# Optimization experiments

Hardware: AMD Instinct MI355X
Metric: run time of the kernel (lower is better)

## Reference

```python
import jax, jax.numpy as jnp
import numpy as np

S, B, C = 7, 2, 20          # YOLOv1 grid / boxes / classes
NE = B * 5 + C              # 30 channels per cell
BATCH = 32768
NBOX = 4                    # ground-truth boxes per image
L_COORD = 5.0


def _encode_np(boxes, classes):
    """Vectorized numpy replica of YoloLoss.encode, including its quirks:
    conf written at channel 4 + S*k (=> 4 and 11), class at channel 10 which is
    then overwritten by wh_y*S via the s+2:s+4 slice for k=1 (s=7 -> 9:11).
    boxes: [N, nb, 4] in xyxy, classes: [N, nb] int."""
    N, nb = classes.shape
    t = np.zeros((N, S, S, NE), np.float32)
    wh = boxes[:, :, 2:] - boxes[:, :, :2]
    cxcy = (boxes[:, :, 2:] + boxes[:, :, :2]) / 2.0
    cell = 1.0 / S
    ij = np.ceil(cxcy / cell) - 1.0                 # [N, nb, 2] (col, row)
    ijc = np.clip(ij, 0, S - 1).astype(np.int64)
    img = np.repeat(np.arange(N), nb)
    col = ijc[:, :, 0].ravel()
    row = ijc[:, :, 1].ravel()
    whf = (wh * S).reshape(-1, 2).astype(np.float32)
    delta = ((cxcy - ij * cell) / cell).reshape(-1, 2).astype(np.float32)
    cls = classes.ravel().astype(np.float32)
    t[img, row, col, 4] = 1.0          # conf, k=0 (4 + S*0)
    t[img, row, col, 11] = 1.0         # conf, k=1 (4 + S*1)
    t[img, row, col, 10] = cls         # class id (will be clobbered below)
    t[img, row, col, 2:4] = whf        # k=0 wh
    t[img, row, col, 0:2] = delta      # k=0 xy
    t[img, row, col, 9:11] = whf       # k=1 wh -- overwrites channel 10!
    t[img, row, col, 7:9] = delta      # k=1 xy
    return t.reshape(N, S * S, NE)


def setup_inputs() -> dict:
    key = jax.random.key(0)
    prediction = jax.random.normal(key, (BATCH, S * S, NE), dtype=jnp.float32)
    rng = np.random.default_rng(0)
    cxcy = rng.uniform(0.15, 0.85, (BATCH, NBOX, 2)).astype(np.float32)
    wh = rng.uniform(0.05, 0.3, (BATCH, NBOX, 2)).astype(np.float32)
    boxes = np.concatenate([cxcy - wh / 2, cxcy + wh / 2], axis=-1)  # xyxy
    classes = rng.integers(0, C, (BATCH, NBOX))
    target = jnp.asarray(_encode_np(boxes, classes))
    return {"prediction": prediction, "target": target}


def _point_form(b):
    # cxcywh -> xyxy on last axis
    return jnp.concatenate([b[..., :2] - b[..., 2:4] / 2,
                            b[..., :2] + b[..., 2:4] / 2], axis=-1)


def _iou(a, b):
    # a: [..., Bp, 4], b: [..., Bt, 4] (xyxy) -> [..., Bp, Bt]
    a = a[..., :, None, :]
    b = b[..., None, :, :]
    lo = jnp.maximum(a[..., :2], b[..., :2])
    hi = jnp.minimum(a[..., 2:], b[..., 2:])
    inter = jnp.prod(jnp.clip(hi - lo, 0.0, None), axis=-1)
    area_a = jnp.prod(a[..., 2:] - a[..., :2], axis=-1)
    area_b = jnp.prod(b[..., 2:] - b[..., :2], axis=-1)
    return inter / (area_a + area_b - inter + 1e-12)


def reference(prediction, target):
    coord = target[:, :, 4] > 0                         # [N, G] cells with objects
    bp = prediction[:, :, :B * 5].reshape(*prediction.shape[:2], B, 5)
    bt = target[:, :, :B * 5].reshape(*target.shape[:2], B, 5)

    # responsible-box matching: iou[bp_i, bt_j], argmax over predicted boxes per target box
    iou = _iou(_point_form(bp[..., :4]), _point_form(bt[..., :4]))  # [N,G,Bp,Bt]
    idx = jnp.argmax(iou, axis=-2)                                  # [N,G,Bt]
    resp = (jax.nn.one_hot(idx, B, dtype=jnp.float32).sum(-2) > 0)  # dedup, [N,G,B]
    resp = resp & coord[..., None]
    resp_f = resp.astype(jnp.float32)
    cnt = jnp.maximum(resp_f.sum(), 1.0)

    # containment loss: BCE-with-logits, mean over responsible boxes
    conf_p = bp[..., 4]
    conf_t = bt[..., 4]
    bce = jnp.logaddexp(0.0, conf_p) - conf_p * conf_t
    contain_loss = jnp.sum(bce * resp_f) / cnt

    # localization loss: mean MSE on xy + mean MSE on wh over responsible boxes
    sq_xy = (bp[..., 0:2] - bt[..., 0:2]) ** 2
    sq_wh = (bp[..., 2:4] - bt[..., 2:4]) ** 2
    loc_loss = (jnp.sum(sq_xy * resp_f[..., None]) / (2.0 * cnt)
                + jnp.sum(sq_wh * resp_f[..., None]) / (2.0 * cnt))

    # class loss: cross-entropy, mean over object cells
    logits = prediction[:, :, B * 5:]                               # [N,G,C]
    cls = jnp.clip(jnp.floor(target[:, :, B * 5]), 0, C - 1).astype(jnp.int32)
    lsm = jax.nn.log_softmax(logits, axis=-1)
    nll = -jnp.take_along_axis(lsm, cls[..., None], axis=-1)[..., 0]
    coord_f = coord.astype(jnp.float32)
    class_loss = jnp.sum(nll * coord_f) / jnp.maximum(coord_f.sum(), 1.0)

    # NOTE: original also computes l_noobj * noobj MSE into total_loss but then
    # returns class + contain + l_coord*loc, so noobj is dead code.
    return class_loss + contain_loss + L_COORD * loc_loss
```

## Files before the change

kernel.cpp:

```cpp
#include <hip/hip_runtime.h>
#include <math.h>

#define NCELL (32768 * 49)
#define NE 30
#define NC 20
#define G1 1568
#define BLK 256
#define CPB 1024


__device__ __forceinline__ void process_cell(
    const float* __restrict__ pred, const float* __restrict__ targ, int cell,
    float& a0, float& a1, float& a2, float& a3, float& a4, float& a5) {

    const float2* p2 = reinterpret_cast<const float2*>(pred + (size_t)cell * NE);
    const float2* t2 = reinterpret_cast<const float2*>(targ + (size_t)cell * NE);

    float p[30], t[12];
    #pragma unroll
    for (int i = 0; i < 15; ++i) { float2 v = p2[i]; p[2*i] = v.x; p[2*i+1] = v.y; }
    #pragma unroll
    for (int i = 0; i < 6; ++i)  { float2 v = t2[i]; t[2*i] = v.x; t[2*i+1] = v.y; }

    float iou[2][2];
    #pragma unroll
    for (int i = 0; i < 2; ++i) {
        const float pcx = p[5*i], pcy = p[5*i+1], pw = p[5*i+2], ph = p[5*i+3];
        const float alx = pcx - pw*0.5f, aly = pcy - ph*0.5f;
        const float ahx = pcx + pw*0.5f, ahy = pcy + ph*0.5f;
        const float area_a = pw * ph;
        #pragma unroll
        for (int j = 0; j < 2; ++j) {
            const float tcx = t[5*j], tcy = t[5*j+1], tw = t[5*j+2], th = t[5*j+3];
            const float blx = tcx - tw*0.5f, bly = tcy - th*0.5f;
            const float bhx = tcx + tw*0.5f, bhy = tcy + th*0.5f;
            float ix = fminf(ahx, bhx) - fmaxf(alx, blx);
            float iy = fminf(ahy, bhy) - fmaxf(aly, bly);
            ix = fmaxf(ix, 0.f); iy = fmaxf(iy, 0.f);
            const float inter = ix * iy;
            const float area_b = tw * th;
            iou[i][j] = inter / (area_a + area_b - inter + 1e-12f);
        }
    }
    const int idx0 = (iou[1][0] > iou[0][0]) ? 1 : 0;
    const int idx1 = (iou[1][1] > iou[0][1]) ? 1 : 0;

    #pragma unroll
    for (int k = 0; k < 2; ++k) {
        const bool resp = (idx0 == k || idx1 == k);
        if (resp) {
            a0 += 1.f;
            const float cp = p[5*k+4], ct = t[5*k+4];
            a1 += fmaxf(cp, 0.f) + log1pf(expf(-fabsf(cp))) - cp * ct;
            const float dx = p[5*k]   - t[5*k];
            const float dy = p[5*k+1] - t[5*k+1];
            a2 += dx*dx + dy*dy;
            const float dw = p[5*k+2] - t[5*k+2];
            const float dh = p[5*k+3] - t[5*k+3];
            a3 += dw*dw + dh*dh;
        }
    }

    a5 += 1.f;
    const float cf = fminf(fmaxf(floorf(t[10]), 0.f), 19.f);
    const int cls = (int)cf;
    float m = p[10];
    #pragma unroll
    for (int c = 1; c < NC; ++c) m = fmaxf(m, p[10 + c]);
    float se = 0.f;
    float sel = 0.f;
    #pragma unroll
    for (int c = 0; c < NC; ++c) {
        se += expf(p[10 + c] - m);
        sel += (c == cls) ? p[10 + c] : 0.f;
    }
    a4 += -(sel - m - logf(se));
}

__global__ __launch_bounds__(BLK) void yolo_partial(
    const float* __restrict__ pred,
    const float* __restrict__ targ,
    float* __restrict__ partial) {

    const int base = blockIdx.x * CPB;
    const int tid  = threadIdx.x;
    const int wave = tid >> 6;
    const int lane = tid & 63;

    float t4v[4];
    #pragma unroll
    for (int k = 0; k < 4; ++k)
        t4v[k] = targ[(size_t)(base + k * BLK + tid) * NE + 4];

    __shared__ int s_idx[4][256];
    __shared__ int s_cnt[4];
    int cnt = 0;
    #pragma unroll
    for (int k = 0; k < 4; ++k) {
        const bool c = t4v[k] > 0.f;
        const unsigned long long m = __ballot(c);
        const int pre = __popcll(m & ((1ull << lane) - 1ull));
        if (c) s_idx[wave][cnt + pre] = k * BLK + tid;
        cnt += __popcll(m);
    }
    if (lane == 0) s_cnt[wave] = cnt;
    __syncthreads();

    const int c0 = s_cnt[0], c1 = s_cnt[1], c2 = s_cnt[2], c3 = s_cnt[3];
    const int total = c0 + c1 + c2 + c3;

    float a0 = 0.f, a1 = 0.f, a2 = 0.f, a3 = 0.f, a4 = 0.f, a5 = 0.f;

    for (int i = tid; i < total; i += BLK) {
        int j = i, w = 0;
        if (j >= c0) { j -= c0; w = 1;
            if (j >= c1) { j -= c1; w = 2;
                if (j >= c2) { j -= c2; w = 3; } } }
        const int loc = s_idx[w][j];
        process_cell(pred, targ, base + loc, a0, a1, a2, a3, a4, a5);
    }

    #pragma unroll
    for (int off = 32; off > 0; off >>= 1) {
        a0 += __shfl_down(a0, off, 64);
        a1 += __shfl_down(a1, off, 64);
        a2 += __shfl_down(a2, off, 64);
        a3 += __shfl_down(a3, off, 64);
        a4 += __shfl_down(a4, off, 64);
        a5 += __shfl_down(a5, off, 64);
    }

    __shared__ float sm[4][6];
    if (lane == 0) {
        sm[wave][0] = a0; sm[wave][1] = a1; sm[wave][2] = a2;
        sm[wave][3] = a3; sm[wave][4] = a4; sm[wave][5] = a5;
    }
    __syncthreads();
    if (tid == 0) {
        #pragma unroll
        for (int k = 0; k < 6; ++k) {
            float s = sm[0][k] + sm[1][k] + sm[2][k] + sm[3][k];
            partial[blockIdx.x * 6 + k] = s;
        }
    }
}

__global__ __launch_bounds__(BLK) void yolo_final(
    const float* __restrict__ partial, float* __restrict__ out) {
    __shared__ double sm[BLK][6];
    double a[6] = {0, 0, 0, 0, 0, 0};
    for (int i = threadIdx.x; i < G1; i += BLK) {
        #pragma unroll
        for (int k = 0; k < 6; ++k) a[k] += (double)partial[i * 6 + k];
    }
    #pragma unroll
    for (int k = 0; k < 6; ++k) sm[threadIdx.x][k] = a[k];
    __syncthreads();
    for (int off = BLK / 2; off > 0; off >>= 1) {
        if (threadIdx.x < off) {
            #pragma unroll
            for (int k = 0; k < 6; ++k) sm[threadIdx.x][k] += sm[threadIdx.x + off][k];
        }
        __syncthreads();
    }
    if (threadIdx.x == 0) {
        const double resp_sum  = sm[0][0];
        const double bce_sum   = sm[0][1];
        const double sqxy_sum  = sm[0][2];
        const double sqwh_sum  = sm[0][3];
        const double nll_sum   = sm[0][4];
        const double coord_sum = sm[0][5];
        const double cnt = fmax(resp_sum, 1.0);
        const double contain_loss = bce_sum / cnt;
        const double loc_loss = (sqxy_sum + sqwh_sum) / (2.0 * cnt);
        const double class_loss = nll_sum / fmax(coord_sum, 1.0);
        out[0] = (float)(class_loss + contain_loss + 5.0 * loc_loss);
    }
}

extern "C" void kernel_launch(void* const* d_in, const int* in_sizes, int n_in,
                              void* d_out, int out_size, void* d_ws, size_t ws_size,
                              hipStream_t stream) {
    const float* pred = (const float*)d_in[0];
    const float* targ = (const float*)d_in[1];
    float* partial = (float*)d_ws;

    yolo_partial<<<G1, BLK, 0, stream>>>(pred, targ, partial);
    yolo_final<<<1, BLK, 0, stream>>>(partial, (float*)d_out);
}
```

Before: 49.03 us.

## Fuse final reduction into main kernel via last-block atomic counter

Merges the two-kernel partial/final reduction into one kernel: each block stores its partial sums, increments a global counter, and the last block to arrive performs the double-precision final reduction. It also halves the cells per block and doubles the grid for more parallelism and smaller shared index arrays. This removes a second kernel launch in exchange for an extra memset, an atomic per block, and a serial tail in the last block over twice as many partials.

```diff
diff --git a/kernel.cpp b/kernel.cpp
--- a/kernel.cpp
+++ b/kernel.cpp
@@ -4,9 +4,9 @@
 #define NCELL (32768 * 49)
 #define NE 30
 #define NC 20
-#define G1 1568
 #define BLK 256
-#define CPB 1024
+#define CPB 512
+#define G1 3136
 
 
 __device__ __forceinline__ void process_cell(
@@ -77,30 +77,36 @@
     a4 += -(sel - m - logf(se));
 }
 
-__global__ __launch_bounds__(BLK) void yolo_partial(
+__global__ __launch_bounds__(BLK) void yolo_fused(
     const float* __restrict__ pred,
     const float* __restrict__ targ,
-    float* __restrict__ partial) {
+    unsigned int* __restrict__ counter,
+    float* __restrict__ partial,
+    float* __restrict__ out) {
 
     const int base = blockIdx.x * CPB;
     const int tid  = threadIdx.x;
     const int wave = tid >> 6;
     const int lane = tid & 63;
 
-    float t4v[4];
-    #pragma unroll
-    for (int k = 0; k < 4; ++k)
-        t4v[k] = targ[(size_t)(base + k * BLK + tid) * NE + 4];
-
-    __shared__ int s_idx[4][256];
+    float t4a = targ[(size_t)(base + tid)       * NE + 4];
+    float t4b = targ[(size_t)(base + BLK + tid) * NE + 4];
+
+    __shared__ int s_idx[4][128];
     __shared__ int s_cnt[4];
     int cnt = 0;
-    #pragma unroll
-    for (int k = 0; k < 4; ++k) {
-        const bool c = t4v[k] > 0.f;
+    {
+        const bool c = t4a > 0.f;
         const unsigned long long m = __ballot(c);
         const int pre = __popcll(m & ((1ull << lane) - 1ull));
-        if (c) s_idx[wave][cnt + pre] = k * BLK + tid;
+        if (c) s_idx[wave][pre] = tid;
+        cnt = __popcll(m);
+    }
+    {
+        const bool c = t4b > 0.f;
+        const unsigned long long m = __ballot(c);
+        const int pre = __popcll(m & ((1ull << lane) - 1ull));
+        if (c) s_idx[wave][cnt + pre] = BLK + tid;
         cnt += __popcll(m);
     }
     if (lane == 0) s_cnt[wave] = cnt;
@@ -116,8 +122,7 @@
         if (j >= c0) { j -= c0; w = 1;
             if (j >= c1) { j -= c1; w = 2;
                 if (j >= c2) { j -= c2; w = 3; } } }
-        const int loc = s_idx[w][j];
-        process_cell(pred, targ, base + loc, a0, a1, a2, a3, a4, a5);
+        process_cell(pred, targ, base + s_idx[w][j], a0, a1, a2, a3, a4, a5);
     }
 
     #pragma unroll
@@ -131,6 +136,7 @@
     }
 
     __shared__ float sm[4][6];
+    __shared__ int s_is_last;
     if (lane == 0) {
         sm[wave][0] = a0; sm[wave][1] = a1; sm[wave][2] = a2;
         sm[wave][3] = a3; sm[wave][4] = a4; sm[wave][5] = a5;
@@ -140,41 +146,47 @@
         #pragma unroll
         for (int k = 0; k < 6; ++k) {
             float s = sm[0][k] + sm[1][k] + sm[2][k] + sm[3][k];
-            partial[blockIdx.x * 6 + k] = s;
-        }
-    }
-}
-
-__global__ __launch_bounds__(BLK) void yolo_final(
-    const float* __restrict__ partial, float* __restrict__ out) {
-    __shared__ double sm[BLK][6];
-    double a[6] = {0, 0, 0, 0, 0, 0};
-    for (int i = threadIdx.x; i < G1; i += BLK) {
+            __hip_atomic_store(&partial[blockIdx.x * 6 + k], s,
+                               __ATOMIC_RELAXED, __HIP_MEMORY_SCOPE_AGENT);
+        }
+        unsigned int old = __hip_atomic_fetch_add(counter, 1u,
+                               __ATOMIC_ACQ_REL, __HIP_MEMORY_SCOPE_AGENT);
+        s_is_last = (old == (unsigned int)(G1 - 1));
+    }
+    __syncthreads();
+
+    if (s_is_last) {
+        double a[6] = {0, 0, 0, 0, 0, 0};
+        for (int i = tid; i < G1; i += BLK) {
+            #pragma unroll
+            for (int k = 0; k < 6; ++k)
+                a[k] += (double)__hip_atomic_load(&partial[i * 6 + k],
+                            __ATOMIC_RELAXED, __HIP_MEMORY_SCOPE_AGENT);
+        }
+        __shared__ double sd[BLK][6];
         #pragma unroll
-        for (int k = 0; k < 6; ++k) a[k] += (double)partial[i * 6 + k];
-    }
-    #pragma unroll
-    for (int k = 0; k < 6; ++k) sm[threadIdx.x][k] = a[k];
-    __syncthreads();
-    for (int off = BLK / 2; off > 0; off >>= 1) {
-        if (threadIdx.x < off) {
-            #pragma unroll
-            for (int k = 0; k < 6; ++k) sm[threadIdx.x][k] += sm[threadIdx.x + off][k];
-        }
+        for (int k = 0; k < 6; ++k) sd[tid][k] = a[k];
         __syncthreads();
-    }
-    if (threadIdx.x == 0) {
-        const double resp_sum  = sm[0][0];
-        const double bce_sum   = sm[0][1];
-        const double sqxy_sum  = sm[0][2];
-        const double sqwh_sum  = sm[0][3];
-        const double nll_sum   = sm[0][4];
-        const double coord_sum = sm[0][5];
-        const double cnt = fmax(resp_sum, 1.0);
-        const double contain_loss = bce_sum / cnt;
-        const double loc_loss = (sqxy_sum + sqwh_sum) / (2.0 * cnt);
-        const double class_loss = nll_sum / fmax(coord_sum, 1.0);
-        out[0] = (float)(class_loss + contain_loss + 5.0 * loc_loss);
+        for (int off = BLK / 2; off > 0; off >>= 1) {
+            if (tid < off) {
+                #pragma unroll
+                for (int k = 0; k < 6; ++k) sd[tid][k] += sd[tid + off][k];
+            }
+            __syncthreads();
+        }
+        if (tid == 0) {
+            const double resp_sum  = sd[0][0];
+            const double bce_sum   = sd[0][1];
+            const double sqxy_sum  = sd[0][2];
+            const double sqwh_sum  = sd[0][3];
+            const double nll_sum   = sd[0][4];
+            const double coord_sum = sd[0][5];
+            const double cnt_d = fmax(resp_sum, 1.0);
+            const double contain_loss = bce_sum / cnt_d;
+            const double loc_loss = (sqxy_sum + sqwh_sum) / (2.0 * cnt_d);
+            const double class_loss = nll_sum / fmax(coord_sum, 1.0);
+            out[0] = (float)(class_loss + contain_loss + 5.0 * loc_loss);
+        }
     }
 }
 
@@ -183,8 +195,9 @@
                               hipStream_t stream) {
     const float* pred = (const float*)d_in[0];
     const float* targ = (const float*)d_in[1];
-    float* partial = (float*)d_ws;
-
-    yolo_partial<<<G1, BLK, 0, stream>>>(pred, targ, partial);
-    yolo_final<<<1, BLK, 0, stream>>>(partial, (float*)d_out);
+    unsigned int* counter = (unsigned int*)d_ws;
+    float* partial = (float*)((char*)d_ws + 256);
+
+    hipMemsetAsync(d_ws, 0, 256, stream);
+    yolo_fused<<<G1, BLK, 0, stream>>>(pred, targ, counter, partial, (float*)d_out);
 }
```

After: 108.1 us. 121% more time.
